# Kernel tuning notes

Measured on AMD Instinct MI355X. Metric: run time of the kernel, lower is better.

Reference implementation:

```python
import jax, jax.numpy as jnp
import numpy as np
from jax import lax

# Geometry constants (stand-in for beijing* globals)
A = 96           # beijingAngleNum
P = 4            # beijingPlanes
DET0, DET1 = 256, 8   # beijingSubDetectorSize [u, v]
NZ, NY, NX = 32, 256, 256  # beijingVolumeSize (nz = P * DET1)
T = 256          # ray integration steps
LAMB = 0.01


def _bilinear(vol, ix, iy):
    # vol: [nz, ny, nx]; ix, iy: [...] index-space coords. Zero outside.
    nz, ny, nx = vol.shape
    x0 = jnp.floor(ix); y0 = jnp.floor(iy)
    fx = (ix - x0).astype(vol.dtype); fy = (iy - y0).astype(vol.dtype)
    x0i = x0.astype(jnp.int32); y0i = y0.astype(jnp.int32)

    def g(yi, xi):
        valid = ((xi >= 0) & (xi < nx) & (yi >= 0) & (yi < ny)).astype(vol.dtype)
        v = vol[:, jnp.clip(yi, 0, ny - 1), jnp.clip(xi, 0, nx - 1)]  # [nz, ...]
        return v * valid

    return (g(y0i, x0i) * (1 - fy) * (1 - fx)
            + g(y0i, x0i + 1) * (1 - fy) * fx
            + g(y0i + 1, x0i) * fy * (1 - fx)
            + g(y0i + 1, x0i + 1) * fy * fx)


def forward_project(vol):
    # vol: [NZ, NY, NX] -> sinogram [A, NZ, DET0], parallel-beam over 180 deg
    angles = jnp.arange(A, dtype=jnp.float32) * (np.pi / A)
    u = jnp.arange(DET0, dtype=jnp.float32) - (DET0 - 1) / 2.0  # detector coord
    t = jnp.arange(T, dtype=jnp.float32) - (T - 1) / 2.0        # along-ray coord

    def per_angle(_, th):
        c, s = jnp.cos(th), jnp.sin(th)
        x = -u[:, None] * s + t[None, :] * c   # [DET0, T]
        y = u[:, None] * c + t[None, :] * s
        samp = _bilinear(vol, x + (NX - 1) / 2.0, y + (NY - 1) / 2.0)  # [NZ,DET0,T]
        return None, samp.sum(-1)  # line integral, [NZ, DET0]

    _, S = lax.scan(per_angle, None, angles)
    return S  # [A, NZ, DET0]


def back_project(S):
    # S: [A, NZ, DET0] -> volume [NZ, NY, NX] (adjoint-style backprojection)
    angles = jnp.arange(A, dtype=jnp.float32) * (np.pi / A)
    yy = jnp.arange(NY, dtype=jnp.float32) - (NY - 1) / 2.0
    xx = jnp.arange(NX, dtype=jnp.float32) - (NX - 1) / 2.0
    Y, X = jnp.meshgrid(yy, xx, indexing='ij')  # [NY, NX]

    def per_angle(acc, inp):
        th, Sa = inp  # Sa: [NZ, DET0]
        c, s = jnp.cos(th), jnp.sin(th)
        ub = -X * s + Y * c + (DET0 - 1) / 2.0  # detector bin coord [NY,NX]
        u0 = jnp.floor(ub)
        fu = (ub - u0).astype(Sa.dtype)
        u0i = u0.astype(jnp.int32)

        def g(ui):
            valid = ((ui >= 0) & (ui < DET0)).astype(Sa.dtype)
            return Sa[:, jnp.clip(ui, 0, DET0 - 1)] * valid  # [NZ,NY,NX]

        val = g(u0i) * (1 - fu) + g(u0i + 1) * fu
        return acc + val, None

    vol0 = jnp.zeros((NZ, NY, NX), dtype=S.dtype)
    vol, _ = lax.scan(per_angle, vol0, (angles, S))
    return vol


def setup_inputs() -> dict:
    key = jax.random.key(0)
    k1, k2 = jax.random.split(key)
    x = jax.random.normal(k1, (1, 1, NZ, NY, NX), dtype=jnp.float32)
    p = jax.random.normal(k2, (1, 1, A * P, DET1, DET0), dtype=jnp.float32)
    return {"x": x, "p": p}


def reference(x, p):
    vol = x[0, 0]                              # [NZ, NY, NX]
    S = forward_project(vol)                   # [A, NZ, DET0] native
    # ForwardProjection wrapper: (A,P,V,U) -> permute -> flat external layout
    ext = S.reshape(A, P, DET1, DET0).transpose(0, 2, 1, 3).reshape(1, 1, A * P, DET1, DET0)
    residual = ext - p
    # BackProjection wrapper: undo external layout back to native
    res_native = residual.reshape(A, DET1, P, DET0).transpose(0, 2, 1, 3).reshape(A, NZ, DET0)
    volb = back_project(res_native)            # [NZ, NY, NX]
    return (-LAMB * volb)[None, None]          # [1,1,NZ,NY,NX]
```

## Files before the change

kernel.cpp:

```cpp
#include <hip/hip_runtime.h>
#include <hip/hip_fp16.h>

#define A     96
#define DET0  256
#define NZ    32
#define NY    256
#define NX    256
#define T     256
#define LAMB  0.01f

#define TRIG_OFF  0
#define REST_OFF  256
#define VOLB_OFF  786688
#define PART_OFF  1835264
#define RES_ELEMS 786432

__device__ __forceinline__ void accp_mix(float& a0, float& a1, unsigned v, float w) {
    asm("v_fma_mix_f32 %0, %2, %3, %0 op_sel:[0,0,0] op_sel_hi:[1,0,0]\n\t"
        "v_fma_mix_f32 %1, %2, %3, %1 op_sel:[1,0,0] op_sel_hi:[1,0,0]"
        : "+v"(a0), "+v"(a1)
        : "v"(v), "v"(w));
}
__device__ __forceinline__ void acc8h(float* acc, uint4 q, float w) {
    accp_mix(acc[0], acc[1], q.x, w);
    accp_mix(acc[2], acc[3], q.y, w);
    accp_mix(acc[4], acc[5], q.z, w);
    accp_mix(acc[6], acc[7], q.w, w);
}

__global__ __launch_bounds__(256) void k_transpose(const float* __restrict__ src,
                                                   unsigned short* __restrict__ vol_h,
                                                   float* __restrict__ trig,
                                                   const float* __restrict__ p,
                                                   float* __restrict__ res_t) {
    __shared__ float lds[64 * 33];
    const int y   = blockIdx.y;
    const int x0  = blockIdx.x * 64;
    const int tid = threadIdx.x;

    if (blockIdx.x == 0 && y == 0 && tid < A) {
        float th = (float)tid * (float)(3.14159265358979323846 / (double)A);
        trig[2 * tid]     = cosf(th);
        trig[2 * tid + 1] = sinf(th);
    }

    const int xr = tid & 63;
    const int zr = tid >> 6;
    #pragma unroll
    for (int pz = 0; pz < 8; ++pz) {
        int z = pz * 4 + zr;
        lds[xr * 33 + z] = src[(z * NY + y) * NX + x0 + xr];
    }
    __syncthreads();
    const int zw = tid & 31;
    const int xw = tid >> 5;
    #pragma unroll
    for (int px = 0; px < 8; ++px) {
        int xi = px * 8 + xw;
        vol_h[(y * NX + x0 + xi) * NZ + zw] =
            __half_as_ushort(__float2half(lds[xi * 33 + zw]));
    }

    if (y < A) {
        const int a  = y;
        const int u0 = blockIdx.x * 64;
        __syncthreads();
        const int col = tid & 63;
        const int r0  = tid >> 6;
        #pragma unroll
        for (int i = 0; i < 8; ++i) {
            int r = i * 4 + r0;
            lds[r * 65 + col] = p[a * 8192 + r * 256 + u0 + col];
        }
        __syncthreads();
        const int ul = tid >> 2;
        const int zb = (tid & 3) * 8;
        float o[8];
        #pragma unroll
        for (int k = 0; k < 8; ++k) {
            int z = zb + k;
            int r = ((z & 7) << 2) + (z >> 3);
            o[k] = -lds[r * 65 + ul];
        }
        float4* d = (float4*)(res_t + (a * DET0 + u0 + ul) * NZ + zb);
        d[0] = make_float4(o[0], o[1], o[2], o[3]);
        d[1] = make_float4(o[4], o[5], o[6], o[7]);
    }
}

__device__ __forceinline__ void rng(float g, float b, float L, float H,
                                    float& lo, float& hi) {
    if (fabsf(g) > 1e-5f) {
        float r0 = (L - b) / g, r1 = (H - b) / g;
        lo = fminf(r0, r1); hi = fmaxf(r0, r1);
    } else {
        bool in = (b >= L && b <= H);
        lo = in ? -1e9f : 1e9f;
        hi = in ? 1e9f : -1e9f;
    }
}
__device__ __forceinline__ int clampi(float v) {
    return (int)fminf(fmaxf(v, -2.f), 258.f);
}

__device__ __forceinline__ void sample_edge8(const char* base16, int col,
                                             float ix, float iy, float* acc) {
    float xf = floorf(ix), yf = floorf(iy);
    float fx = ix - xf, fy = iy - yf;
    int x  = (int)xf + col;
    int y0 = (int)yf;
    float wx  = col ? fx : (1.f - fx);
    float wy0 = 1.f - fy, wy1 = fy;
    if ((unsigned)x >= NX)        wx  = 0.f;
    if ((unsigned)y0 >= NY)       wy0 = 0.f;
    if ((unsigned)(y0 + 1) >= NY) wy1 = 0.f;
    if (wx == 0.f || (wy0 == 0.f && wy1 == 0.f)) return;
    int cx  = min(max(x, 0), NX - 1);
    int cy0 = min(max(y0, 0), NY - 1);
    int cy1 = min(max(y0 + 1, 0), NY - 1);
    uint4 q0 = *(const uint4*)(base16 + ((size_t)((cy0 << 8) + cx) << 6));
    uint4 q1 = *(const uint4*)(base16 + ((size_t)((cy1 << 8) + cx) << 6));
    acc8h(acc, q0, wy0 * wx);
    acc8h(acc, q1, wy1 * wx);
}

__global__ __launch_bounds__(256) void k_forward(const unsigned short* __restrict__ vol_h,
                                                 const float* __restrict__ trig,
                                                 float* __restrict__ part) {
    const int tid = threadIdx.x;
    const int a   = blockIdx.z;
    const int u   = blockIdx.x * 32 + (tid >> 3);
    const int zq8 = tid & 7;
    const int col = zq8 >> 2;
    const int cid = blockIdx.y;
    const int C   = gridDim.y;

    const float c = trig[2 * a];
    const float s = trig[2 * a + 1];
    const float uu = (float)u - 127.5f;
    const float bx = fmaf(-uu, s, 127.5f);
    const float by = fmaf(uu, c, 127.5f);

    float lo1, hi1, lo2, hi2;
    rng(c, bx, -1.f, 256.f, lo1, hi1);
    rng(s, by, -1.f, 256.f, lo2, hi2);
    float fl = fmaxf(lo1, lo2), fh = fminf(hi1, hi2);
    int F0 = max(0,     clampi(ceilf(fl + 127.5f)));
    int F1 = min(T - 1, clampi(floorf(fh + 127.5f)));
    int len = F1 - F0 + 1; if (len < 0) len = 0;
    int b0 = F0 + (len * cid) / C;
    int b1 = F0 + (len * (cid + 1)) / C - 1;
    rng(c, bx, 1.f, 253.5f, lo1, hi1);
    rng(s, by, 1.f, 253.5f, lo2, hi2);
    float il = fmaxf(lo1, lo2), ih = fminf(hi1, hi2);
    int tI0 = max(clampi(ceilf(il + 127.5f)) + 1, b0);
    int tI1 = min(clampi(floorf(ih + 127.5f)) - 1, b1);
    if (tI0 > tI1) { tI0 = b1 + 1; tI1 = b1; }

    const char* base16 = (const char*)vol_h + (zq8 & 3) * 16;
    const char* base2  = (const char*)vol_h + zq8 * 16;
    float acc[8];
    #pragma unroll
    for (int k = 0; k < 8; ++k) acc[k] = 0.f;

    for (int t = b0; t < tI0; ++t) {
        float ttf = (float)t - 127.5f;
        sample_edge8(base16, col, fmaf(ttf, c, bx), fmaf(ttf, s, by), acc);
    }
    for (int t = tI0; t <= tI1; ++t) {
        float ttf = (float)t - 127.5f;
        float ix = fmaf(ttf, c, bx);
        float iy = fmaf(ttf, s, by);
        float xf = floorf(ix), yf = floorf(iy);
        float fx = ix - xf, fy = iy - yf;
        int row = ((int)yf << 8) + (int)xf;
        const char* p0 = base2 + ((size_t)row << 6);
        uint4 q_top = *(const uint4*)(p0);
        uint4 q_bot = *(const uint4*)(p0 + 16384);
        float wx = col ? fx : (1.f - fx);
        acc8h(acc, q_top, (1.f - fy) * wx);
        acc8h(acc, q_bot, fy * wx);
    }
    for (int t = tI1 + 1; t <= b1; ++t) {
        float ttf = (float)t - 127.5f;
        sample_edge8(base16, col, fmaf(ttf, c, bx), fmaf(ttf, s, by), acc);
    }

    #pragma unroll
    for (int k = 0; k < 8; ++k) acc[k] += __shfl_xor(acc[k], 4);

    if (col == 0) {
        float4* dst = (float4*)(part + (size_t)cid * RES_ELEMS +
                                ((a * DET0 + u) * NZ + (zq8 & 3) * 8));
        dst[0] = make_float4(acc[0], acc[1], acc[2], acc[3]);
        dst[1] = make_float4(acc[4], acc[5], acc[6], acc[7]);
    }
}

__global__ __launch_bounds__(256) void k_combine(const float* __restrict__ part,
                                                 float* __restrict__ res_t,
                                                 int C) {
    const int j4 = blockIdx.x * 256 + threadIdx.x;
    float4 v = ((const float4*)res_t)[j4];
    for (int c = 0; c < C; ++c) {
        float4 w = ((const float4*)(part + (size_t)c * RES_ELEMS))[j4];
        v.x += w.x; v.y += w.y; v.z += w.z; v.w += w.w;
    }
    ((float4*)res_t)[j4] = v;
}

__global__ __launch_bounds__(256, 8) void k_backward(const float* __restrict__ res_t,
                                                     const float* __restrict__ trig,
                                                     float* __restrict__ out) {
    __shared__ float ob[32 * 33];
    const int tid = threadIdx.x;
    const int y  = blockIdx.y;
    const int xb = blockIdx.x * 32;
    const int xs = tid >> 3;
    const int zq = tid & 7;
    const char* rbase = (const char*)res_t + zq * 16;
    const float xx = (float)(xb + xs) - 127.5f;
    const float yy = (float)y - 127.5f;

    float4 acc = make_float4(0.f, 0.f, 0.f, 0.f);
    #pragma unroll 4
    for (int a = 0; a < A; ++a) {
        float cc = trig[2 * a];
        float ss = trig[2 * a + 1];
        float ub = fmaf(-xx, ss, fmaf(yy, cc, 127.5f));
        float uf = floorf(ub);
        float fu = ub - uf;
        int i0 = (int)uf;
        float w0 = ((unsigned)i0 < DET0) ? (1.f - fu) : 0.f;
        float w1 = ((unsigned)(i0 + 1) < DET0) ? fu : 0.f;
        int c1 = min(max(i0 + 1, 0), DET0);
        int off = ((a * DET0 + c1) * NZ - NZ) << 2;
        float4 v0 = *(const float4*)(rbase + off);
        float4 v1 = *(const float4*)(rbase + off + 128);
        acc.x = fmaf(w0, v0.x, fmaf(w1, v1.x, acc.x));
        acc.y = fmaf(w0, v0.y, fmaf(w1, v1.y, acc.y));
        acc.z = fmaf(w0, v0.z, fmaf(w1, v1.z, acc.z));
        acc.w = fmaf(w0, v0.w, fmaf(w1, v1.w, acc.w));
    }

    ob[(zq * 4 + 0) * 33 + xs] = acc.x;
    ob[(zq * 4 + 1) * 33 + xs] = acc.y;
    ob[(zq * 4 + 2) * 33 + xs] = acc.z;
    ob[(zq * 4 + 3) * 33 + xs] = acc.w;
    __syncthreads();

    const int z  = tid >> 3;
    const int x4 = (tid & 7) * 4;
    float4 o = make_float4(ob[z * 33 + x4],     ob[z * 33 + x4 + 1],
                           ob[z * 33 + x4 + 2], ob[z * 33 + x4 + 3]);
    float4* dst = (float4*)(out + (size_t)z * (NY * NX) + y * NX + xb + x4);
    *dst = make_float4(-LAMB * o.x, -LAMB * o.y, -LAMB * o.z, -LAMB * o.w);
}

extern "C" void kernel_launch(void* const* d_in, const int* in_sizes, int n_in,
                              void* d_out, int out_size, void* d_ws, size_t ws_size,
                              hipStream_t stream) {
    const float* x = (const float*)d_in[0];
    const float* p = (const float*)d_in[1];
    float* out = (float*)d_out;
    float* ws  = (float*)d_ws;

    float*          trig  = ws + TRIG_OFF;
    float*          res_t = ws + REST_OFF;
    unsigned short* vol_h = (unsigned short*)(ws + VOLB_OFF);
    float*          part  = ws + PART_OFF;

    size_t avail = ws_size / 4;
    int C = 8;
    while (C > 1 && (size_t)PART_OFF + (size_t)C * RES_ELEMS > avail) C >>= 1;

    k_transpose<<<dim3(NX / 64, NY), 256, 0, stream>>>(x, vol_h, trig, p, res_t);
    k_forward  <<<dim3(8, C, A), 256, 0, stream>>>(vol_h, trig, part);
    k_combine  <<<dim3(RES_ELEMS / 4 / 256), 256, 0, stream>>>(part, res_t, C);
    k_backward <<<dim3(NX / 32, NY), 256, 0, stream>>>(res_t, trig, out);
}
```

Baseline: 185.1 us.

## Drop ray-split partials and combine kernel; accumulate forward directly into residual

```diff
diff --git a/kernel.cpp b/kernel.cpp
--- a/kernel.cpp
+++ b/kernel.cpp
@@ -12,7 +12,6 @@
 #define TRIG_OFF  0
 #define REST_OFF  256
 #define VOLB_OFF  786688
-#define PART_OFF  1835264
 #define RES_ELEMS 786432
 
 __device__ __forceinline__ void accp_mix(float& a0, float& a1, unsigned v, float w) {
@@ -124,16 +123,14 @@
     acc8h(acc, q1, wy1 * wx);
 }
 
-__global__ __launch_bounds__(256) void k_forward(const unsigned short* __restrict__ vol_h,
+__global__ __launch_bounds__(128) void k_forward(const unsigned short* __restrict__ vol_h,
                                                  const float* __restrict__ trig,
-                                                 float* __restrict__ part) {
+                                                 float* __restrict__ res_t) {
     const int tid = threadIdx.x;
-    const int a   = blockIdx.z;
-    const int u   = blockIdx.x * 32 + (tid >> 3);
+    const int a   = blockIdx.y;
+    const int u   = blockIdx.x * 16 + (tid >> 3);
     const int zq8 = tid & 7;
     const int col = zq8 >> 2;
-    const int cid = blockIdx.y;
-    const int C   = gridDim.y;
 
     const float c = trig[2 * a];
     const float s = trig[2 * a + 1];
@@ -145,11 +142,8 @@
     rng(c, bx, -1.f, 256.f, lo1, hi1);
     rng(s, by, -1.f, 256.f, lo2, hi2);
     float fl = fmaxf(lo1, lo2), fh = fminf(hi1, hi2);
-    int F0 = max(0,     clampi(ceilf(fl + 127.5f)));
-    int F1 = min(T - 1, clampi(floorf(fh + 127.5f)));
-    int len = F1 - F0 + 1; if (len < 0) len = 0;
-    int b0 = F0 + (len * cid) / C;
-    int b1 = F0 + (len * (cid + 1)) / C - 1;
+    int b0 = max(0,     clampi(ceilf(fl + 127.5f)));
+    int b1 = min(T - 1, clampi(floorf(fh + 127.5f)));
     rng(c, bx, 1.f, 253.5f, lo1, hi1);
     rng(s, by, 1.f, 253.5f, lo2, hi2);
     float il = fmaxf(lo1, lo2), ih = fminf(hi1, hi2);
@@ -190,23 +184,11 @@
     for (int k = 0; k < 8; ++k) acc[k] += __shfl_xor(acc[k], 4);
 
     if (col == 0) {
-        float4* dst = (float4*)(part + (size_t)cid * RES_ELEMS +
-                                ((a * DET0 + u) * NZ + (zq8 & 3) * 8));
-        dst[0] = make_float4(acc[0], acc[1], acc[2], acc[3]);
-        dst[1] = make_float4(acc[4], acc[5], acc[6], acc[7]);
-    }
-}
-
-__global__ __launch_bounds__(256) void k_combine(const float* __restrict__ part,
-                                                 float* __restrict__ res_t,
-                                                 int C) {
-    const int j4 = blockIdx.x * 256 + threadIdx.x;
-    float4 v = ((const float4*)res_t)[j4];
-    for (int c = 0; c < C; ++c) {
-        float4 w = ((const float4*)(part + (size_t)c * RES_ELEMS))[j4];
-        v.x += w.x; v.y += w.y; v.z += w.z; v.w += w.w;
-    }
-    ((float4*)res_t)[j4] = v;
+        float4* dst = (float4*)(res_t + ((a * DET0 + u) * NZ + (zq8 & 3) * 8));
+        float4 s0 = dst[0], s1 = dst[1];
+        dst[0] = make_float4(s0.x + acc[0], s0.y + acc[1], s0.z + acc[2], s0.w + acc[3]);
+        dst[1] = make_float4(s1.x + acc[4], s1.y + acc[5], s1.z + acc[6], s1.w + acc[7]);
+    }
 }
 
 __global__ __launch_bounds__(256, 8) void k_backward(const float* __restrict__ res_t,
@@ -268,14 +250,8 @@
     float*          trig  = ws + TRIG_OFF;
     float*          res_t = ws + REST_OFF;
     unsigned short* vol_h = (unsigned short*)(ws + VOLB_OFF);
-    float*          part  = ws + PART_OFF;
-
-    size_t avail = ws_size / 4;
-    int C = 8;
-    while (C > 1 && (size_t)PART_OFF + (size_t)C * RES_ELEMS > avail) C >>= 1;
 
     k_transpose<<<dim3(NX / 64, NY), 256, 0, stream>>>(x, vol_h, trig, p, res_t);
-    k_forward  <<<dim3(8, C, A), 256, 0, stream>>>(vol_h, trig, part);
-    k_combine  <<<dim3(RES_ELEMS / 4 / 256), 256, 0, stream>>>(part, res_t, C);
+    k_forward  <<<dim3(16, A), 128, 0, stream>>>(vol_h, trig, res_t);
     k_backward <<<dim3(NX / 32, NY), 256, 0, stream>>>(res_t, trig, out);
 }
```

After: 262.9 us. +42.0%, slower.
